# Kernel optimization log

Measured on AMD Instinct MI355X. Metric: run time of the kernel, lower is better.

The kernel has to match this reference:

```python
import jax, jax.numpy as jnp
import numpy as np

DIM = 1024
DIM_HEAD = 64
HEADS = 16
DIM_INNER = DIM_HEAD * HEADS  # 1024


def setup_inputs() -> dict:
    key = jax.random.key(0)
    k1, k2, k3 = jax.random.split(key, 3)
    b, n = 2, 2048
    x = jax.random.normal(k1, (b, n, DIM), dtype=jnp.float32)
    gamma = jnp.ones((DIM,), dtype=jnp.float32)
    # torch Linear weight [out,in] applied as x @ W.T; store pre-transposed [in,out]
    w_qkv = jax.random.normal(k2, (DIM, 3 * DIM_INNER), dtype=jnp.float32) * (DIM ** -0.5)
    w_out = jax.random.normal(k3, (DIM_INNER, DIM), dtype=jnp.float32) * (DIM_INNER ** -0.5)
    return {"x": x, "gamma": gamma, "w_qkv": w_qkv, "w_out": w_out}


def reference(x, gamma, w_qkv, w_out):
    h, d = HEADS, DIM_HEAD
    scale = d ** -0.5
    rms_scale = DIM ** 0.5
    # RMSNorm: F.normalize(x, dim=-1) * sqrt(dim) * gamma  (eps=1e-12 clamp on L2 norm)
    norm = jnp.maximum(jnp.linalg.norm(x, axis=-1, keepdims=True), 1e-12)
    xn = x / norm * rms_scale * gamma
    b, n, _ = x.shape
    qkv = xn @ w_qkv  # [b, n, 3*h*d]
    qkv = qkv.reshape(b, n, 3, h, d)
    q = qkv[:, :, 0].transpose(0, 2, 1, 3) * scale  # [b, h, n, d]
    k = qkv[:, :, 1].transpose(0, 2, 1, 3)
    v = qkv[:, :, 2].transpose(0, 2, 1, 3)
    sim = jnp.einsum('bhid,bhjd->bhij', q, k)  # [b, h, n, n]
    causal_mask = jnp.triu(jnp.ones((n, n), dtype=bool), k=1)
    neg = -jnp.finfo(sim.dtype).max
    sim = jnp.where(causal_mask, neg, sim)
    attn = jax.nn.softmax(sim, axis=-1)
    out = jnp.einsum('bhij,bhjd->bhid', attn, v)  # [b, h, n, d]
    out = out.transpose(0, 2, 1, 3).reshape(b, n, h * d)
    return out @ w_out
```

## Files before the change

kernel.cpp:

```cpp
#include <hip/hip_runtime.h>
#include <hip/hip_bf16.h>

typedef __bf16 bf16x8 __attribute__((ext_vector_type(8)));
typedef short s16x4 __attribute__((ext_vector_type(4)));
typedef float f32x4 __attribute__((ext_vector_type(4)));
typedef unsigned short u16x8 __attribute__((ext_vector_type(8)));

#define MFMA_K32(a, b, c) __builtin_amdgcn_mfma_f32_16x16x32_bf16(a, b, c, 0, 0, 0)

static __device__ __forceinline__ f32x4 mfma_k16(s16x4 a, s16x4 b, f32x4 c) {
#ifdef __HIP_DEVICE_COMPILE__
    return __builtin_amdgcn_mfma_f32_16x16x16bf16_1k(a, b, c, 0, 0, 0);
#else
    return c;
#endif
}

static __device__ __forceinline__ float fast_exp2(float x) {
#ifdef __HIP_DEVICE_COMPILE__
    return __builtin_amdgcn_exp2f(x);
#else
    return x;
#endif
}

#define GLL16(gp, lp)                                              \
    __builtin_amdgcn_global_load_lds(                              \
        (const __attribute__((address_space(1))) void*)(gp),       \
        (__attribute__((address_space(3))) void*)(lp), 16, 0, 0)

static __device__ __forceinline__ unsigned short f2bf(float f) {
    unsigned int u = __float_as_uint(f);
    u += 0x7fffu + ((u >> 16) & 1u);
    return (unsigned short)(u >> 16);
}

static __device__ __forceinline__ unsigned int cvtpk_bf16(float lo, float hi) {
#if defined(__HIP_DEVICE_COMPILE__) && __has_builtin(__builtin_amdgcn_cvt_pk_bf16_f32)
    typedef __bf16 bf16x2 __attribute__((ext_vector_type(2)));
    bf16x2 r = __builtin_amdgcn_cvt_pk_bf16_f32(lo, hi);
    return __builtin_bit_cast(unsigned int, r);
#else
    return (unsigned int)f2bf(lo) | ((unsigned int)f2bf(hi) << 16);
#endif
}

#define LOG2E 1.44269504088896340736f

__global__ __launch_bounds__(256) void prep_k(
    const float* __restrict__ x, const float* __restrict__ gamma,
    const float* __restrict__ w_qkv, const float* __restrict__ w_out,
    unsigned short* __restrict__ xn, unsigned short* __restrict__ wtq,
    unsigned short* __restrict__ wto) {
    __shared__ float sm[32][33];
    int bid = blockIdx.x, tid = threadIdx.x;
    if (bid < 4096) {
        const float* in;
        unsigned short* out;
        int R = 1024, C, bx, by;
        if (bid < 3072) { in = w_qkv; out = wtq; C = 3072; bx = bid % 96; by = bid / 96; }
        else { int b2 = bid - 3072; in = w_out; out = wto; C = 1024; bx = b2 % 32; by = b2 / 32; }
        int c0 = bx * 32, r0 = by * 32;
        int tr = tid >> 5, tc = tid & 31;
#pragma unroll
        for (int i = 0; i < 4; i++)
            sm[tr + i * 8][tc] = in[(size_t)(r0 + tr + i * 8) * C + c0 + tc];
        __syncthreads();
#pragma unroll
        for (int i = 0; i < 4; i++)
            out[(size_t)(c0 + tr + i * 8) * R + r0 + tc] = f2bf(sm[tc][tr + i * 8]);
    } else {
        int row = bid - 4096;
        const float* xr = x + (size_t)row * 1024;
        float4 v = *(const float4*)(xr + tid * 4);
        float ss = v.x * v.x + v.y * v.y + v.z * v.z + v.w * v.w;
#pragma unroll
        for (int off = 1; off < 64; off <<= 1) ss += __shfl_xor(ss, off, 64);
        if ((tid & 63) == 0) sm[0][tid >> 6] = ss;
        __syncthreads();
        float tot = sm[0][0] + sm[0][1] + sm[0][2] + sm[0][3];
        float f = 32.0f / fmaxf(sqrtf(tot), 1e-12f);
        float4 g = *(const float4*)(gamma + tid * 4);
        uint2 o;
        o.x = cvtpk_bf16(v.x * f * g.x, v.y * f * g.y);
        o.y = cvtpk_bf16(v.z * f * g.z, v.w * f * g.w);
        *(uint2*)(xn + (size_t)row * 1024 + tid * 4) = o;
    }
}

template <int MODE, int BM>
__global__ __launch_bounds__(256) void gemm_bt_k(
    const unsigned short* __restrict__ A, const unsigned short* __restrict__ BT,
    float* __restrict__ C, unsigned short* __restrict__ qw,
    unsigned short* __restrict__ kw, unsigned short* __restrict__ vw,
    int M, int N, int K) {
    constexpr int RT = 4;
    constexpr int CT = (BM == 128) ? 4 : 2;
    __shared__ unsigned short As[BM][32];
    __shared__ unsigned short Bs[128][32];
    int tid = threadIdx.x;
    int wave = tid >> 6, lane = tid & 63, quad = lane >> 4, l16 = lane & 15;
    int wrb, wcb;
    if constexpr (BM == 128) { wrb = (wave >> 1) * 64; wcb = (wave & 1) * 64; }
    else { wrb = 0; wcb = wave * 32; }
    int m0 = blockIdx.y * BM, n0 = blockIdx.x * 128;
    int lrow = lane >> 2, lcol = (lane & 3) * 8;
    const unsigned short *Ag0, *Ag1 = nullptr;
    if constexpr (BM == 128) {
        Ag0 = A + (size_t)(m0 + wave * 32 + lrow) * K + lcol;
        Ag1 = A + (size_t)(m0 + wave * 32 + 16 + lrow) * K + lcol;
    } else {
        Ag0 = A + (size_t)(m0 + wave * 16 + lrow) * K + lcol;
    }
    const unsigned short* Bg0 = BT + (size_t)(n0 + wave * 32 + lrow) * K + lcol;
    const unsigned short* Bg1 = BT + (size_t)(n0 + wave * 32 + 16 + lrow) * K + lcol;
    f32x4 acc[RT][CT] = {};
    for (int k0 = 0; k0 < K; k0 += 32) {
        __syncthreads();
        if constexpr (BM == 128) {
            GLL16(Ag0 + k0, &As[wave * 32][0]);
            GLL16(Ag1 + k0, &As[wave * 32 + 16][0]);
        } else {
            GLL16(Ag0 + k0, &As[wave * 16][0]);
        }
        GLL16(Bg0 + k0, &Bs[wave * 32][0]);
        GLL16(Bg1 + k0, &Bs[wave * 32 + 16][0]);
        __syncthreads();
        bf16x8 af[RT], bfr[CT];
#pragma unroll
        for (int t = 0; t < RT; t++)
            af[t] = *(const bf16x8*)&As[wrb + t * 16 + l16][quad * 8];
#pragma unroll
        for (int t = 0; t < CT; t++)
            bfr[t] = *(const bf16x8*)&Bs[wcb + t * 16 + l16][quad * 8];
#pragma unroll
        for (int rt = 0; rt < RT; rt++)
#pragma unroll
            for (int ct = 0; ct < CT; ct++)
                acc[rt][ct] = MFMA_K32(af[rt], bfr[ct], acc[rt][ct]);
    }
#pragma unroll
    for (int rt = 0; rt < RT; rt++) {
        int mb = m0 + wrb + rt * 16 + quad * 4;
        int b = mb >> 11, nn = mb & 2047;
#pragma unroll
        for (int ct = 0; ct < CT; ct++) {
            int col = n0 + wcb + ct * 16 + l16;
            if (MODE == 0) {
#pragma unroll
                for (int r = 0; r < 4; r++)
                    C[(size_t)(mb + r) * N + col] = acc[rt][ct][r];
            } else {
                int sec = col >> 10, ci = col & 1023;
                int hh = ci >> 6, dd = ci & 63;
                int bh = b * 16 + hh;
                if (sec == 0) {
#pragma unroll
                    for (int r = 0; r < 4; r++)
                        qw[((size_t)bh * 2048 + nn + r) * 64 + dd] =
                            f2bf(acc[rt][ct][r] * (0.125f * LOG2E));
                } else if (sec == 1) {
#pragma unroll
                    for (int r = 0; r < 4; r++)
                        kw[((size_t)bh * 2048 + nn + r) * 64 + dd] = f2bf(acc[rt][ct][r]);
                } else {
                    uint2 pk;
                    pk.x = cvtpk_bf16(acc[rt][ct][0], acc[rt][ct][1]);
                    pk.y = cvtpk_bf16(acc[rt][ct][2], acc[rt][ct][3]);
                    *(uint2*)&vw[((size_t)bh * 64 + dd) * 2048 + nn] = pk;
                }
            }
        }
    }
}

__global__ __launch_bounds__(256) void attn_k(
    const unsigned short* __restrict__ q, const unsigned short* __restrict__ k,
    const unsigned short* __restrict__ vt, unsigned short* __restrict__ o) {
    __shared__ unsigned short Ks[2][64][72];
    __shared__ unsigned short Vt[2][64][72];
    int bh = blockIdx.y, px = blockIdx.x;
    int tid = threadIdx.x, wave = tid >> 6, lane = tid & 63;
    int quad = lane >> 4, l16 = lane & 15;
    int b = bh >> 4, h = bh & 15;
    const unsigned short* qg = q + (size_t)bh * 2048 * 64;
    const unsigned short* kg = k + (size_t)bh * 2048 * 64;
    const unsigned short* vg = vt + (size_t)bh * 64 * 2048;
    int srow = tid >> 2, scol = (tid & 3) * 16;
    u16x8 pk0, pk1, pv0, pv1;
#pragma unroll 1
    for (int phase = 0; phase < 2; phase++) {
        int qt = phase == 0 ? (31 - px) : px;
        int q0w = qt * 64 + wave * 16;
        bf16x8 bq[2];
#pragma unroll
        for (int ks = 0; ks < 2; ks++)
            bq[ks] = *(const bf16x8*)&qg[(size_t)(q0w + l16) * 64 + ks * 32 + quad * 8];
        f32x4 ot[4] = {};
        float mrun = -1e38f, lrun = 0.f;
        int nkt = qt + 1;
        {
            const unsigned short* kp = kg + (size_t)srow * 64 + scol;
            pk0 = *(const u16x8*)kp;
            pk1 = *(const u16x8*)(kp + 8);
            const unsigned short* vp = vg + (size_t)srow * 2048 + scol;
            pv0 = *(const u16x8*)vp;
            pv1 = *(const u16x8*)(vp + 8);
            *(u16x8*)&Ks[0][srow][scol] = pk0;
            *(u16x8*)&Ks[0][srow][scol + 8] = pk1;
            *(u16x8*)&Vt[0][srow][scol] = pv0;
            *(u16x8*)&Vt[0][srow][scol + 8] = pv1;
        }
        __syncthreads();
        for (int kt = 0; kt < nkt; kt++) {
            int cb = kt & 1;
            bool pf = (kt + 1 < nkt);
            if (pf) {
                const unsigned short* kp = kg + (size_t)((kt + 1) * 64 + srow) * 64 + scol;
                pk0 = *(const u16x8*)kp;
                pk1 = *(const u16x8*)(kp + 8);
                const unsigned short* vp = vg + (size_t)srow * 2048 + (kt + 1) * 64 + scol;
                pv0 = *(const u16x8*)vp;
                pv1 = *(const u16x8*)(vp + 8);
            }
            f32x4 sf[4];
#pragma unroll
            for (int ct = 0; ct < 4; ct++) {
                bf16x8 ak0 = *(const bf16x8*)&Ks[cb][ct * 16 + l16][quad * 8];
                bf16x8 ak1 = *(const bf16x8*)&Ks[cb][ct * 16 + l16][32 + quad * 8];
                f32x4 s = {};
                s = MFMA_K32(ak0, bq[0], s);
                s = MFMA_K32(ak1, bq[1], s);
                sf[ct] = s;
            }
            if (kt == qt) {
                int qloc = wave * 16 + l16;
#pragma unroll
                for (int ct = 0; ct < 4; ct++)
#pragma unroll
                    for (int r = 0; r < 4; r++)
                        if (ct * 16 + quad * 4 + r > qloc) sf[ct][r] = -1e30f;
            }
            float mx = -1e30f;
#pragma unroll
            for (int ct = 0; ct < 4; ct++)
#pragma unroll
                for (int r = 0; r < 4; r++) mx = fmaxf(mx, sf[ct][r]);
            mx = fmaxf(mx, __shfl_xor(mx, 16, 64));
            mx = fmaxf(mx, __shfl_xor(mx, 32, 64));
            float mnew = fmaxf(mrun, mx);
            float al = fast_exp2(mrun - mnew);
            mrun = mnew;
            float rs = 0.f;
#pragma unroll
            for (int ct = 0; ct < 4; ct++)
#pragma unroll
                for (int r = 0; r < 4; r++) {
                    float p = fast_exp2(sf[ct][r] - mnew);
                    sf[ct][r] = p;
                    rs += p;
                }
            rs += __shfl_xor(rs, 16, 64);
            rs += __shfl_xor(rs, 32, 64);
            lrun = lrun * al + rs;
            s16x4 bpr[4];
#pragma unroll
            for (int ct = 0; ct < 4; ct++) {
                uint2 u;
                u.x = cvtpk_bf16(sf[ct][0], sf[ct][1]);
                u.y = cvtpk_bf16(sf[ct][2], sf[ct][3]);
                bpr[ct] = __builtin_bit_cast(s16x4, u);
            }
#pragma unroll
            for (int dt = 0; dt < 4; dt++) {
#pragma unroll
                for (int r = 0; r < 4; r++) ot[dt][r] *= al;
#pragma unroll
                for (int ct = 0; ct < 4; ct++) {
                    s16x4 av = *(const s16x4*)&Vt[cb][dt * 16 + l16][ct * 16 + quad * 4];
                    ot[dt] = mfma_k16(av, bpr[ct], ot[dt]);
                }
            }
            if (pf) {
                *(u16x8*)&Ks[1 - cb][srow][scol] = pk0;
                *(u16x8*)&Ks[1 - cb][srow][scol + 8] = pk1;
                *(u16x8*)&Vt[1 - cb][srow][scol] = pv0;
                *(u16x8*)&Vt[1 - cb][srow][scol + 8] = pv1;
            }
            __syncthreads();
        }
        float inv = 1.0f / lrun;
        size_t rowbase = ((size_t)b * 2048 + q0w + l16) * 1024 + h * 64;
#pragma unroll
        for (int dt = 0; dt < 4; dt++) {
            uint2 pk;
            pk.x = cvtpk_bf16(ot[dt][0] * inv, ot[dt][1] * inv);
            pk.y = cvtpk_bf16(ot[dt][2] * inv, ot[dt][3] * inv);
            *(uint2*)&o[rowbase + dt * 16 + quad * 4] = pk;
        }
    }
}

extern "C" void kernel_launch(void* const* d_in, const int* in_sizes, int n_in,
                              void* d_out, int out_size, void* d_ws, size_t ws_size,
                              hipStream_t stream) {
    const float* x = (const float*)d_in[0];
    const float* gamma = (const float*)d_in[1];
    const float* w_qkv = (const float*)d_in[2];
    const float* w_out = (const float*)d_in[3];
    float* out = (float*)d_out;
    char* ws = (char*)d_ws;

    unsigned short* xn = (unsigned short*)(ws);
    unsigned short* wtq = (unsigned short*)(ws + 8388608);
    unsigned short* wto = (unsigned short*)(ws + 14680064);
    unsigned short* qw = (unsigned short*)(ws + 16777216);
    unsigned short* kw = (unsigned short*)(ws + 25165824);
    unsigned short* vw = (unsigned short*)(ws + 33554432);
    unsigned short* ao = xn;

    prep_k<<<8192, 256, 0, stream>>>(x, gamma, w_qkv, w_out, xn, wtq, wto);
    gemm_bt_k<1, 128><<<dim3(24, 32), 256, 0, stream>>>(xn, wtq, nullptr, qw, kw, vw,
                                                        4096, 3072, 1024);
    attn_k<<<dim3(16, 32), 256, 0, stream>>>(qw, kw, vw, ao);
    gemm_bt_k<0, 64><<<dim3(8, 64), 256, 0, stream>>>(ao, wto, out, nullptr, nullptr,
                                                      nullptr, 4096, 1024, 1024);
}
```

Before: 195.4 us.

## Split attention key dimension across waves with shared-memory softmax merge

Each wave now takes a 16-key slice of every 64-key tile and covers all 64 queries, instead of owning 16 queries against all keys. Per-wave running max and sum are merged through shared memory at the end, and the partial outputs are reduced across waves in a tree before one wave writes them. Output rescaling is skipped when no row max changed. This cuts the per-wave LDS reads of K and V, but it quadruples the accumulator registers and adds reduction passes and barriers.

```diff
diff --git a/kernel.cpp b/kernel.cpp
--- a/kernel.cpp
+++ b/kernel.cpp
@@ -177,8 +177,10 @@
 __global__ __launch_bounds__(256) void attn_k(
     const unsigned short* __restrict__ q, const unsigned short* __restrict__ k,
     const unsigned short* __restrict__ vt, unsigned short* __restrict__ o) {
-    __shared__ unsigned short Ks[2][64][72];
-    __shared__ unsigned short Vt[2][64][72];
+    __shared__ __align__(16) char smem[36864];
+    __shared__ float Msh[4][64], Lsh[4][64];
+    unsigned short* KsB = (unsigned short*)smem;
+    unsigned short* VtB = (unsigned short*)(smem + 18432);
     int bh = blockIdx.y, px = blockIdx.x;
     int tid = threadIdx.x, wave = tid >> 6, lane = tid & 63;
     int quad = lane >> 4, l16 = lane & 15;
@@ -191,13 +193,18 @@
 #pragma unroll 1
     for (int phase = 0; phase < 2; phase++) {
         int qt = phase == 0 ? (31 - px) : px;
-        int q0w = qt * 64 + wave * 16;
-        bf16x8 bq[2];
-#pragma unroll
-        for (int ks = 0; ks < 2; ks++)
-            bq[ks] = *(const bf16x8*)&qg[(size_t)(q0w + l16) * 64 + ks * 32 + quad * 8];
-        f32x4 ot[4] = {};
-        float mrun = -1e38f, lrun = 0.f;
+        int q0 = qt * 64;
+        bf16x8 bq[4][2];
+#pragma unroll
+        for (int ct = 0; ct < 4; ct++)
+#pragma unroll
+            for (int ks = 0; ks < 2; ks++)
+                bq[ct][ks] = *(const bf16x8*)&qg[(size_t)(q0 + ct * 16 + l16) * 64 +
+                                                 ks * 32 + quad * 8];
+        f32x4 ot[4][4] = {};
+        float mrun[4], lrun[4];
+#pragma unroll
+        for (int ct = 0; ct < 4; ct++) { mrun[ct] = -1e38f; lrun[ct] = 0.f; }
         int nkt = qt + 1;
         {
             const unsigned short* kp = kg + (size_t)srow * 64 + scol;
@@ -206,10 +213,10 @@
             const unsigned short* vp = vg + (size_t)srow * 2048 + scol;
             pv0 = *(const u16x8*)vp;
             pv1 = *(const u16x8*)(vp + 8);
-            *(u16x8*)&Ks[0][srow][scol] = pk0;
-            *(u16x8*)&Ks[0][srow][scol + 8] = pk1;
-            *(u16x8*)&Vt[0][srow][scol] = pv0;
-            *(u16x8*)&Vt[0][srow][scol + 8] = pv1;
+            *(u16x8*)&KsB[srow * 72 + scol] = pk0;
+            *(u16x8*)&KsB[srow * 72 + scol + 8] = pk1;
+            *(u16x8*)&VtB[srow * 72 + scol] = pv0;
+            *(u16x8*)&VtB[srow * 72 + scol + 8] = pv1;
         }
         __syncthreads();
         for (int kt = 0; kt < nkt; kt++) {
@@ -223,46 +230,59 @@
                 pv0 = *(const u16x8*)vp;
                 pv1 = *(const u16x8*)(vp + 8);
             }
+            const unsigned short* Ks = KsB + cb * 4608;
+            const unsigned short* Vc = VtB + cb * 4608;
+            bf16x8 ak0 = *(const bf16x8*)&Ks[(wave * 16 + l16) * 72 + quad * 8];
+            bf16x8 ak1 = *(const bf16x8*)&Ks[(wave * 16 + l16) * 72 + 32 + quad * 8];
             f32x4 sf[4];
 #pragma unroll
             for (int ct = 0; ct < 4; ct++) {
-                bf16x8 ak0 = *(const bf16x8*)&Ks[cb][ct * 16 + l16][quad * 8];
-                bf16x8 ak1 = *(const bf16x8*)&Ks[cb][ct * 16 + l16][32 + quad * 8];
                 f32x4 s = {};
-                s = MFMA_K32(ak0, bq[0], s);
-                s = MFMA_K32(ak1, bq[1], s);
+                s = MFMA_K32(ak0, bq[ct][0], s);
+                s = MFMA_K32(ak1, bq[ct][1], s);
                 sf[ct] = s;
             }
             if (kt == qt) {
-                int qloc = wave * 16 + l16;
-#pragma unroll
-                for (int ct = 0; ct < 4; ct++)
+                int keyb = wave * 16 + quad * 4;
+#pragma unroll
+                for (int ct = 0; ct < 4; ct++) {
+                    int qloc = ct * 16 + l16;
 #pragma unroll
                     for (int r = 0; r < 4; r++)
-                        if (ct * 16 + quad * 4 + r > qloc) sf[ct][r] = -1e30f;
-            }
-            float mx = -1e30f;
-#pragma unroll
-            for (int ct = 0; ct < 4; ct++)
-#pragma unroll
-                for (int r = 0; r < 4; r++) mx = fmaxf(mx, sf[ct][r]);
-            mx = fmaxf(mx, __shfl_xor(mx, 16, 64));
-            mx = fmaxf(mx, __shfl_xor(mx, 32, 64));
-            float mnew = fmaxf(mrun, mx);
-            float al = fast_exp2(mrun - mnew);
-            mrun = mnew;
-            float rs = 0.f;
-#pragma unroll
-            for (int ct = 0; ct < 4; ct++)
+                        if (keyb + r > qloc) sf[ct][r] = -1e30f;
+                }
+            }
+            float al[4];
+            int need = 0;
+#pragma unroll
+            for (int ct = 0; ct < 4; ct++) {
+                float mx = fmaxf(fmaxf(sf[ct][0], sf[ct][1]),
+                                 fmaxf(sf[ct][2], sf[ct][3]));
+                mx = fmaxf(mx, __shfl_xor(mx, 16, 64));
+                mx = fmaxf(mx, __shfl_xor(mx, 32, 64));
+                float mnew = fmaxf(mrun[ct], mx);
+                al[ct] = fast_exp2(mrun[ct] - mnew);
+                mrun[ct] = mnew;
+                float rs = 0.f;
 #pragma unroll
                 for (int r = 0; r < 4; r++) {
                     float p = fast_exp2(sf[ct][r] - mnew);
                     sf[ct][r] = p;
                     rs += p;
                 }
-            rs += __shfl_xor(rs, 16, 64);
-            rs += __shfl_xor(rs, 32, 64);
-            lrun = lrun * al + rs;
+                rs += __shfl_xor(rs, 16, 64);
+                rs += __shfl_xor(rs, 32, 64);
+                lrun[ct] = lrun[ct] * al[ct] + rs;
+                need |= (al[ct] < 1.0f);
+            }
+            if (__any(need)) {
+#pragma unroll
+                for (int dt = 0; dt < 4; dt++)
+#pragma unroll
+                    for (int ct = 0; ct < 4; ct++)
+#pragma unroll
+                        for (int r = 0; r < 4; r++) ot[dt][ct][r] *= al[ct];
+            }
             s16x4 bpr[4];
 #pragma unroll
             for (int ct = 0; ct < 4; ct++) {
@@ -273,31 +293,89 @@
             }
 #pragma unroll
             for (int dt = 0; dt < 4; dt++) {
-#pragma unroll
-                for (int r = 0; r < 4; r++) ot[dt][r] *= al;
-#pragma unroll
-                for (int ct = 0; ct < 4; ct++) {
-                    s16x4 av = *(const s16x4*)&Vt[cb][dt * 16 + l16][ct * 16 + quad * 4];
-                    ot[dt] = mfma_k16(av, bpr[ct], ot[dt]);
+                s16x4 av = *(const s16x4*)&Vc[(dt * 16 + l16) * 72 + wave * 16 + quad * 4];
+#pragma unroll
+                for (int ct = 0; ct < 4; ct++)
+                    ot[dt][ct] = mfma_k16(av, bpr[ct], ot[dt][ct]);
+            }
+            if (pf) {
+                unsigned short* Kn = KsB + (1 - cb) * 4608;
+                unsigned short* Vn = VtB + (1 - cb) * 4608;
+                *(u16x8*)&Kn[srow * 72 + scol] = pk0;
+                *(u16x8*)&Kn[srow * 72 + scol + 8] = pk1;
+                *(u16x8*)&Vn[srow * 72 + scol] = pv0;
+                *(u16x8*)&Vn[srow * 72 + scol + 8] = pv1;
+            }
+            __syncthreads();
+        }
+        if (quad == 0) {
+#pragma unroll
+            for (int ct = 0; ct < 4; ct++) {
+                Msh[wave][ct * 16 + l16] = mrun[ct];
+                Lsh[wave][ct * 16 + l16] = lrun[ct];
+            }
+        }
+        __syncthreads();
+        float fw[4];
+#pragma unroll
+        for (int ct = 0; ct < 4; ct++) {
+            int qq = ct * 16 + l16;
+            float m0 = Msh[0][qq], m1 = Msh[1][qq], m2 = Msh[2][qq], m3 = Msh[3][qq];
+            float mt = fmaxf(fmaxf(m0, m1), fmaxf(m2, m3));
+            float lt = fast_exp2(m0 - mt) * Lsh[0][qq] + fast_exp2(m1 - mt) * Lsh[1][qq] +
+                       fast_exp2(m2 - mt) * Lsh[2][qq] + fast_exp2(m3 - mt) * Lsh[3][qq];
+            fw[ct] = fast_exp2(mrun[ct] - mt) / lt;
+        }
+#pragma unroll
+        for (int dt = 0; dt < 4; dt++)
+#pragma unroll
+            for (int ct = 0; ct < 4; ct++)
+#pragma unroll
+                for (int r = 0; r < 4; r++) ot[dt][ct][r] *= fw[ct];
+        float* OshA = (float*)smem;
+        float* OshB = (float*)(smem + 17408);
+        if (wave & 1) {
+            float* O = (wave == 1) ? OshA : OshB;
+#pragma unroll
+            for (int ct = 0; ct < 4; ct++)
+#pragma unroll
+                for (int dt = 0; dt < 4; dt++)
+                    *(f32x4*)&O[(ct * 16 + l16) * 68 + dt * 16 + quad * 4] = ot[dt][ct];
+        }
+        __syncthreads();
+        if (!(wave & 1)) {
+            float* O = (wave == 0) ? OshA : OshB;
+#pragma unroll
+            for (int ct = 0; ct < 4; ct++)
+#pragma unroll
+                for (int dt = 0; dt < 4; dt++)
+                    ot[dt][ct] += *(const f32x4*)&O[(ct * 16 + l16) * 68 + dt * 16 + quad * 4];
+        }
+        if (wave == 2) {
+#pragma unroll
+            for (int ct = 0; ct < 4; ct++)
+#pragma unroll
+                for (int dt = 0; dt < 4; dt++)
+                    *(f32x4*)&OshB[(ct * 16 + l16) * 68 + dt * 16 + quad * 4] = ot[dt][ct];
+        }
+        __syncthreads();
+        if (wave == 0) {
+#pragma unroll
+            for (int ct = 0; ct < 4; ct++) {
+#pragma unroll
+                for (int dt = 0; dt < 4; dt++)
+                    ot[dt][ct] += *(const f32x4*)&OshB[(ct * 16 + l16) * 68 + dt * 16 + quad * 4];
+                size_t rowbase = ((size_t)b * 2048 + q0 + ct * 16 + l16) * 1024 + h * 64;
+#pragma unroll
+                for (int dt = 0; dt < 4; dt++) {
+                    uint2 pk;
+                    pk.x = cvtpk_bf16(ot[dt][ct][0], ot[dt][ct][1]);
+                    pk.y = cvtpk_bf16(ot[dt][ct][2], ot[dt][ct][3]);
+                    *(uint2*)&o[rowbase + dt * 16 + quad * 4] = pk;
                 }
             }
-            if (pf) {
-                *(u16x8*)&Ks[1 - cb][srow][scol] = pk0;
-                *(u16x8*)&Ks[1 - cb][srow][scol + 8] = pk1;
-                *(u16x8*)&Vt[1 - cb][srow][scol] = pv0;
-                *(u16x8*)&Vt[1 - cb][srow][scol + 8] = pv1;
-            }
-            __syncthreads();
-        }
-        float inv = 1.0f / lrun;
-        size_t rowbase = ((size_t)b * 2048 + q0w + l16) * 1024 + h * 64;
-#pragma unroll
-        for (int dt = 0; dt < 4; dt++) {
-            uint2 pk;
-            pk.x = cvtpk_bf16(ot[dt][0] * inv, ot[dt][1] * inv);
-            pk.y = cvtpk_bf16(ot[dt][2] * inv, ot[dt][3] * inv);
-            *(uint2*)&o[rowbase + dt * 16 + quad * 4] = pk;
-        }
+        }
+        __syncthreads();
     }
 }
 
```

After: 252.5 us. 1.29x slower.

## Restructure attention into single-wave blocks reading K/V directly from global

Applied to the files above, without the earlier changes.

The attention kernel changes from 256-thread blocks that stage K and V tiles in double-buffered shared memory to 64-thread single-wave blocks. Each block handles 32 query rows as two 16-row slices and loads K/V fragments straight from global memory into registers, with no LDS and no barriers. The launch grid grows to 2048 blocks, ordered longest causal chunk first to balance load. In exchange, every wave re-reads K/V from global/L2 with no sharing across waves, so memory traffic and register pressure go up.

```diff
diff --git a/kernel.cpp b/kernel.cpp
--- a/kernel.cpp
+++ b/kernel.cpp
@@ -174,128 +174,123 @@
     }
 }
 
-__global__ __launch_bounds__(256) void attn_k(
+__global__ __launch_bounds__(64) void attn_k(
     const unsigned short* __restrict__ q, const unsigned short* __restrict__ k,
     const unsigned short* __restrict__ vt, unsigned short* __restrict__ o) {
-    __shared__ unsigned short Ks[2][64][72];
-    __shared__ unsigned short Vt[2][64][72];
-    int bh = blockIdx.y, px = blockIdx.x;
-    int tid = threadIdx.x, wave = tid >> 6, lane = tid & 63;
+    int bh = blockIdx.x;
+    int chunk = 63 - (int)blockIdx.y;
+    int lane = threadIdx.x;
     int quad = lane >> 4, l16 = lane & 15;
     int b = bh >> 4, h = bh & 15;
     const unsigned short* qg = q + (size_t)bh * 2048 * 64;
     const unsigned short* kg = k + (size_t)bh * 2048 * 64;
     const unsigned short* vg = vt + (size_t)bh * 64 * 2048;
-    int srow = tid >> 2, scol = (tid & 3) * 16;
-    u16x8 pk0, pk1, pv0, pv1;
+    int q0 = chunk * 32;
+    bf16x8 bq[2][2];
+#pragma unroll
+    for (int s = 0; s < 2; s++)
+#pragma unroll
+        for (int kh = 0; kh < 2; kh++)
+            bq[s][kh] = *(const bf16x8*)&qg[(size_t)(q0 + s * 16 + l16) * 64 +
+                                            kh * 32 + quad * 8];
+    f32x4 ot[4][2] = {};
+    float mrun[2] = {-1e38f, -1e38f}, lrun[2] = {0.f, 0.f};
+    int nkt = (q0 + 31) / 64 + 1;
 #pragma unroll 1
-    for (int phase = 0; phase < 2; phase++) {
-        int qt = phase == 0 ? (31 - px) : px;
-        int q0w = qt * 64 + wave * 16;
-        bf16x8 bq[2];
-#pragma unroll
-        for (int ks = 0; ks < 2; ks++)
-            bq[ks] = *(const bf16x8*)&qg[(size_t)(q0w + l16) * 64 + ks * 32 + quad * 8];
-        f32x4 ot[4] = {};
-        float mrun = -1e38f, lrun = 0.f;
-        int nkt = qt + 1;
-        {
-            const unsigned short* kp = kg + (size_t)srow * 64 + scol;
-            pk0 = *(const u16x8*)kp;
-            pk1 = *(const u16x8*)(kp + 8);
-            const unsigned short* vp = vg + (size_t)srow * 2048 + scol;
-            pv0 = *(const u16x8*)vp;
-            pv1 = *(const u16x8*)(vp + 8);
-            *(u16x8*)&Ks[0][srow][scol] = pk0;
-            *(u16x8*)&Ks[0][srow][scol + 8] = pk1;
-            *(u16x8*)&Vt[0][srow][scol] = pv0;
-            *(u16x8*)&Vt[0][srow][scol + 8] = pv1;
-        }
-        __syncthreads();
-        for (int kt = 0; kt < nkt; kt++) {
-            int cb = kt & 1;
-            bool pf = (kt + 1 < nkt);
-            if (pf) {
-                const unsigned short* kp = kg + (size_t)((kt + 1) * 64 + srow) * 64 + scol;
-                pk0 = *(const u16x8*)kp;
-                pk1 = *(const u16x8*)(kp + 8);
-                const unsigned short* vp = vg + (size_t)srow * 2048 + (kt + 1) * 64 + scol;
-                pv0 = *(const u16x8*)vp;
-                pv1 = *(const u16x8*)(vp + 8);
-            }
-            f32x4 sf[4];
+    for (int kt = 0; kt < nkt; kt++) {
+        const unsigned short* kb = kg + (size_t)(kt * 64) * 64;
+        bf16x8 ak0[4], ak1[4];
+#pragma unroll
+        for (int ct = 0; ct < 4; ct++) {
+            const unsigned short* kr = kb + (size_t)(ct * 16 + l16) * 64;
+            ak0[ct] = *(const bf16x8*)(kr + quad * 8);
+            ak1[ct] = *(const bf16x8*)(kr + 32 + quad * 8);
+        }
+        s16x4 av[4][4];
+#pragma unroll
+        for (int dt = 0; dt < 4; dt++) {
+            const unsigned short* vr = vg + (size_t)(dt * 16 + l16) * 2048 + kt * 64;
+#pragma unroll
+            for (int ct = 0; ct < 4; ct++)
+                av[dt][ct] = *(const s16x4*)(vr + ct * 16 + quad * 4);
+        }
+        f32x4 sf[2][4];
+#pragma unroll
+        for (int s = 0; s < 2; s++)
 #pragma unroll
             for (int ct = 0; ct < 4; ct++) {
-                bf16x8 ak0 = *(const bf16x8*)&Ks[cb][ct * 16 + l16][quad * 8];
-                bf16x8 ak1 = *(const bf16x8*)&Ks[cb][ct * 16 + l16][32 + quad * 8];
-                f32x4 s = {};
-                s = MFMA_K32(ak0, bq[0], s);
-                s = MFMA_K32(ak1, bq[1], s);
-                sf[ct] = s;
-            }
-            if (kt == qt) {
-                int qloc = wave * 16 + l16;
-#pragma unroll
-                for (int ct = 0; ct < 4; ct++)
+                f32x4 t = {};
+                t = MFMA_K32(ak0[ct], bq[s][0], t);
+                t = MFMA_K32(ak1[ct], bq[s][1], t);
+                sf[s][ct] = t;
+            }
+        if (kt == nkt - 1) {
+#pragma unroll
+            for (int s = 0; s < 2; s++) {
+                int qrow = q0 + s * 16 + l16;
+#pragma unroll
+                for (int ct = 0; ct < 4; ct++) {
+                    int key = kt * 64 + ct * 16 + quad * 4;
 #pragma unroll
                     for (int r = 0; r < 4; r++)
-                        if (ct * 16 + quad * 4 + r > qloc) sf[ct][r] = -1e30f;
-            }
+                        if (key + r > qrow) sf[s][ct][r] = -1e30f;
+                }
+            }
+        }
+        s16x4 bpr[2][4];
+        float al[2];
+#pragma unroll
+        for (int s = 0; s < 2; s++) {
             float mx = -1e30f;
 #pragma unroll
             for (int ct = 0; ct < 4; ct++)
 #pragma unroll
-                for (int r = 0; r < 4; r++) mx = fmaxf(mx, sf[ct][r]);
+                for (int r = 0; r < 4; r++) mx = fmaxf(mx, sf[s][ct][r]);
             mx = fmaxf(mx, __shfl_xor(mx, 16, 64));
             mx = fmaxf(mx, __shfl_xor(mx, 32, 64));
-            float mnew = fmaxf(mrun, mx);
-            float al = fast_exp2(mrun - mnew);
-            mrun = mnew;
+            float mnew = fmaxf(mrun[s], mx);
+            al[s] = fast_exp2(mrun[s] - mnew);
+            mrun[s] = mnew;
             float rs = 0.f;
 #pragma unroll
             for (int ct = 0; ct < 4; ct++)
 #pragma unroll
                 for (int r = 0; r < 4; r++) {
-                    float p = fast_exp2(sf[ct][r] - mnew);
-                    sf[ct][r] = p;
+                    float p = fast_exp2(sf[s][ct][r] - mnew);
+                    sf[s][ct][r] = p;
                     rs += p;
                 }
             rs += __shfl_xor(rs, 16, 64);
             rs += __shfl_xor(rs, 32, 64);
-            lrun = lrun * al + rs;
-            s16x4 bpr[4];
+            lrun[s] = lrun[s] * al[s] + rs;
 #pragma unroll
             for (int ct = 0; ct < 4; ct++) {
                 uint2 u;
-                u.x = cvtpk_bf16(sf[ct][0], sf[ct][1]);
-                u.y = cvtpk_bf16(sf[ct][2], sf[ct][3]);
-                bpr[ct] = __builtin_bit_cast(s16x4, u);
-            }
-#pragma unroll
-            for (int dt = 0; dt < 4; dt++) {
-#pragma unroll
-                for (int r = 0; r < 4; r++) ot[dt][r] *= al;
-#pragma unroll
-                for (int ct = 0; ct < 4; ct++) {
-                    s16x4 av = *(const s16x4*)&Vt[cb][dt * 16 + l16][ct * 16 + quad * 4];
-                    ot[dt] = mfma_k16(av, bpr[ct], ot[dt]);
-                }
-            }
-            if (pf) {
-                *(u16x8*)&Ks[1 - cb][srow][scol] = pk0;
-                *(u16x8*)&Ks[1 - cb][srow][scol + 8] = pk1;
-                *(u16x8*)&Vt[1 - cb][srow][scol] = pv0;
-                *(u16x8*)&Vt[1 - cb][srow][scol + 8] = pv1;
-            }
-            __syncthreads();
-        }
-        float inv = 1.0f / lrun;
-        size_t rowbase = ((size_t)b * 2048 + q0w + l16) * 1024 + h * 64;
+                u.x = cvtpk_bf16(sf[s][ct][0], sf[s][ct][1]);
+                u.y = cvtpk_bf16(sf[s][ct][2], sf[s][ct][3]);
+                bpr[s][ct] = __builtin_bit_cast(s16x4, u);
+            }
+        }
+#pragma unroll
+        for (int dt = 0; dt < 4; dt++)
+#pragma unroll
+            for (int s = 0; s < 2; s++) {
+#pragma unroll
+                for (int r = 0; r < 4; r++) ot[dt][s][r] *= al[s];
+#pragma unroll
+                for (int ct = 0; ct < 4; ct++)
+                    ot[dt][s] = mfma_k16(av[dt][ct], bpr[s][ct], ot[dt][s]);
+            }
+    }
+#pragma unroll
+    for (int s = 0; s < 2; s++) {
+        float inv = 1.0f / lrun[s];
+        size_t rowbase = ((size_t)b * 2048 + q0 + s * 16 + l16) * 1024 + h * 64;
 #pragma unroll
         for (int dt = 0; dt < 4; dt++) {
             uint2 pk;
-            pk.x = cvtpk_bf16(ot[dt][0] * inv, ot[dt][1] * inv);
-            pk.y = cvtpk_bf16(ot[dt][2] * inv, ot[dt][3] * inv);
+            pk.x = cvtpk_bf16(ot[dt][s][0] * inv, ot[dt][s][1] * inv);
+            pk.y = cvtpk_bf16(ot[dt][s][2] * inv, ot[dt][s][3] * inv);
             *(uint2*)&o[rowbase + dt * 16 + quad * 4] = pk;
         }
     }
@@ -322,7 +317,7 @@
     prep_k<<<8192, 256, 0, stream>>>(x, gamma, w_qkv, w_out, xn, wtq, wto);
     gemm_bt_k<1, 128><<<dim3(24, 32), 256, 0, stream>>>(xn, wtq, nullptr, qw, kw, vw,
                                                         4096, 3072, 1024);
-    attn_k<<<dim3(16, 32), 256, 0, stream>>>(qw, kw, vw, ao);
+    attn_k<<<dim3(32, 64), 64, 0, stream>>>(qw, kw, vw, ao);
     gemm_bt_k<0, 64><<<dim3(8, 64), 256, 0, stream>>>(ao, wto, out, nullptr, nullptr,
                                                       nullptr, 4096, 1024, 1024);
 }
```

Measured after the change: 247.0 us. 26.4% more time.
